# Optimization experiments

Hardware: AMD Instinct MI355X
Metric: run time of the kernel (lower is better)

## Reference

```python
import jax, jax.numpy as jnp
import numpy as np

N = 8192
D_IN = 512
HID = 1024
EMB = 64
N_EFF = 2
N_CLASSES = 16
MARGIN = 0.01


def setup_inputs() -> dict:
    key = jax.random.key(0)
    ks = jax.random.split(key, 10)
    data = jax.random.normal(ks[0], (N, D_IN), dtype=jnp.float32)
    labels = jax.random.randint(ks[1], (N,), 0, N_CLASSES).astype(jnp.float32)
    x = jnp.concatenate([labels[:, None], data], axis=1)  # [N, 1+D_IN]

    def lin(k, fan_in, fan_out):
        return jax.random.normal(k, (fan_in, fan_out), dtype=jnp.float32) / np.sqrt(fan_in)

    return {
        "x": x,
        "W1": lin(ks[2], D_IN, HID), "b1": jnp.zeros((HID,), jnp.float32),
        "W2": lin(ks[3], HID, EMB), "b2": jnp.zeros((EMB,), jnp.float32),
        "W3": lin(ks[4], EMB, HID), "b3": jnp.zeros((HID,), jnp.float32),
        "W4": lin(ks[5], HID, D_IN), "b4": jnp.zeros((D_IN,), jnp.float32),
    }


def reference(x, W1, b1, W2, b2, W3, b3, W4, b4):
    labels = x[:, 0]
    data = x[:, 1:]

    # encoder / decoder (tanh MLP autoencoder)
    embedding = jnp.tanh(data @ W1 + b1) @ W2 + b2          # [N, EMB]
    decoded = jnp.tanh(embedding @ W3 + b3) @ W4 + b4       # [N, D_IN]

    conserved = embedding[:, N_EFF:]                        # [N, C]
    n_conserved = conserved.shape[1]

    # labels.expand + unique(return_inverse) on row-replicated labels is
    # equivalent to comparing the labels directly.
    lbl = labels.astype(jnp.int32)
    Y = lbl[:, None] != lbl[None, :]                        # [N, N] bool

    # D_mean[i,j] = mean_d (c_i - c_j)^2, via Gram-matrix algebra (one pass,
    # no [N,N,C] intermediate).
    sq = jnp.sum(conserved * conserved, axis=1)             # [N]
    gram = conserved @ conserved.T                          # [N, N]
    D_mean = jnp.maximum(sq[:, None] + sq[None, :] - 2.0 * gram, 0.0) / n_conserved

    Yf = Y.astype(D_mean.dtype)
    n_diff = jnp.sum(Yf)
    C_sim = jnp.sum(Yf * D_mean) / (n_diff + 1.0)
    C_diff = jnp.sum((1.0 - Yf) * jnp.maximum(0.0, MARGIN - D_mean)) / (
        (D_mean.shape[0] * D_mean.shape[1] - n_diff) + 1.0)

    return decoded, C_sim, C_diff
```

## Files before the change

kernel.cpp:

```cpp
#include <hip/hip_runtime.h>
#include <stdint.h>

#define NROWS 8192
#define DIN   512
#define HIDN  1024
#define EMBN  64
#define NCONS 62
#define NCLS  16
#define MARGINF 0.01f
#define NREP  16

typedef unsigned short u16;
typedef __attribute__((ext_vector_type(8))) short short8;
typedef __attribute__((ext_vector_type(4))) float floatx4;

__device__ __forceinline__ u16 f32_to_bf16(float f) {
  union { float f; uint32_t u; } x; x.f = f;
  uint32_t u = x.u;
  uint32_t r = (u + 0x7FFFu + ((u >> 16) & 1u)) >> 16;
  return (u16)r;
}

__device__ __forceinline__ float bf16_to_f32(u16 h) {
  union { uint32_t u; float f; } x; x.u = (uint32_t)h << 16;
  return x.f;
}

__device__ __forceinline__ float fast_tanh(float x) {
  float xc = fminf(fmaxf(x, -10.f), 10.f);
  float e = __expf(2.f * xc);
  return (e - 1.f) * __builtin_amdgcn_rcpf(e + 1.f);
}

__device__ __forceinline__ void load_lds16(const u16* g, u16* l) {
  __builtin_amdgcn_global_load_lds(
      (const __attribute__((address_space(1))) void*)g,
      (__attribute__((address_space(3))) void*)l, 16, 0, 0);
}

__device__ __forceinline__ void pack_tile(const float* __restrict__ W,
                                          u16* __restrict__ Wp,
                                          int N, int KU, int t, int lane)
{
  const int r = lane >> 2, slot = lane & 3;
  const int c = slot ^ ((r >> 1) & 3);
  const int nt = t / KU, ku = t - nt * KU;
  const int n = nt * 16 + r;
  const int kb = ku * 32 + c * 8;
  short8 v;
#pragma unroll
  for (int j = 0; j < 8; ++j) v[j] = (short)f32_to_bf16(W[(size_t)(kb + j) * N + n]);
  *(short8*)(Wp + ((size_t)t * 64 + lane) * 8) = v;
}

__global__ __launch_bounds__(256)
void prep_all(const float* __restrict__ x,
              const float* __restrict__ W1, const float* __restrict__ W2,
              const float* __restrict__ W3, const float* __restrict__ W4,
              u16* __restrict__ A0p, u16* __restrict__ W1p,
              u16* __restrict__ W2p, u16* __restrict__ W3p,
              u16* __restrict__ W4p, float* __restrict__ slab,
              int* __restrict__ labels, int* __restrict__ hist32)
{
  __shared__ int hh[NCLS];
  const int b = blockIdx.x;
  const int tid = threadIdx.x;
  const int tl = tid >> 6, lane = tid & 63;
  if (b < 2048) {
    if (b < 32) {
      if (tid < NCLS) hh[tid] = 0;
      const int row = b * 256 + tid;
      const int lab = (int)x[(size_t)row * 513];
      labels[row] = lab;
      __syncthreads();
      atomicAdd(&hh[lab], 1);
      __syncthreads();
      if (tid < NCLS) hist32[b * NCLS + tid] = hh[tid];
    }
    const int t = b * 4 + tl;
    const int rt = t >> 4, ku = t & 15;
    const int r = lane & 15, q = lane >> 4;
    const float* src = x + (size_t)(rt * 16 + r) * 513 + 1 + ku * 32 + q * 8;
    short8 v;
#pragma unroll
    for (int j = 0; j < 8; ++j) v[j] = (short)f32_to_bf16(src[j]);
    *(short8*)(A0p + ((size_t)t * 64 + lane) * 8) = v;
  } else if (b < 2304) {
    pack_tile(W1, W1p, 1024, 16, (b - 2048) * 4 + tl, lane);
  } else if (b < 2336) {
    pack_tile(W2, W2p, 64, 32, (b - 2304) * 4 + tl, lane);
  } else if (b < 2368) {
    pack_tile(W3, W3p, 1024, 2, (b - 2336) * 4 + tl, lane);
  } else if (b < 2624) {
    pack_tile(W4, W4p, 512, 32, (b - 2368) * 4 + tl, lane);
  } else {
    float* dst = slab + (size_t)(b - 2624) * 4096;
    for (int i = tid; i < 4096; i += 256) dst[i] = 0.f;
  }
}

__global__ __launch_bounds__(512, 4)
void fused123(const u16* __restrict__ A0p, const u16* __restrict__ W1p,
              const float* __restrict__ b1, const u16* __restrict__ W2p,
              const float* __restrict__ b2, const u16* __restrict__ W3p,
              const float* __restrict__ b3,
              const int* __restrict__ labels, const int* __restrict__ hist32,
              int* __restrict__ offs, int* __restrict__ counts,
              int* __restrict__ idx,
              u16* __restrict__ Ebf, float* __restrict__ sqrow,
              float* __restrict__ vsumR, float* __restrict__ SsumR,
              u16* __restrict__ T)
{
  __shared__ u16 uni[16 * 1032];
  __shared__ u16 El[16 * 66];
  __shared__ float lv[NCLS][64];
  __shared__ float lsq[NCLS][64];
  __shared__ int colsum[NCLS], preblk[NCLS], scur[NCLS];

  const int tid = threadIdx.x;

  if (blockIdx.x < 16) {
    const int sb = blockIdx.x;
    if (tid < NCLS) {
      int s = 0, p = 0;
      for (int b2i = 0; b2i < 32; ++b2i) {
        const int h = hist32[b2i * NCLS + tid];
        s += h;
        if (b2i < sb * 2) p += h;
      }
      colsum[tid] = s;
      preblk[tid] = p;
    }
    __syncthreads();
    if (tid < NCLS) {
      int o = 0;
      for (int c = 0; c < tid; ++c) o += colsum[c];
      scur[tid] = o + preblk[tid];
      if (sb == 0) {
        counts[tid] = colsum[tid];
        offs[tid] = o;
        if (tid == NCLS - 1) offs[NCLS] = o + colsum[NCLS - 1];
      }
    }
    __syncthreads();
    {
      const int row = sb * 512 + tid;
      const int p = atomicAdd(&scur[labels[row]], 1);
      idx[p] = row;
    }
    return;
  }

  const int bx = blockIdx.x - 16;
  const int m0 = bx * 16;
  const int rep = blockIdx.x & (NREP - 1);
  const int w = tid >> 6, lane = tid & 63;
  const int quad = lane >> 4, l15 = lane & 15;
  const int lamb = l15 * 4 + (quad ^ ((l15 >> 1) & 3));

  for (int i = tid; i < NCLS * 64; i += 512) {
    ((float*)lv)[i] = 0.f; ((float*)lsq)[i] = 0.f;
  }

  u16* Hc = uni;
  float* Epart = (float*)uni;

  const u16* Wbase = W1p + (size_t)(w * 8) * 16 * 512 + lamb * 8;
  const u16* Abase = A0p + (size_t)(bx * 16) * 512 + lane * 8;

  floatx4 acc1[8];
#pragma unroll
  for (int jj = 0; jj < 8; ++jj) acc1[jj] = (floatx4){0.f, 0.f, 0.f, 0.f};

  short8 bfb[2][8];
  short8 afb[2];
  afb[0] = *(const short8*)(Abase);
#pragma unroll
  for (int jj = 0; jj < 8; ++jj)
    bfb[0][jj] = *(const short8*)(Wbase + (size_t)(jj * 16) * 512);

#pragma unroll
  for (int s = 0; s < 16; ++s) {
    const int cur = s & 1, nxt = cur ^ 1;
    if (s < 15) {
      afb[nxt] = *(const short8*)(Abase + (size_t)(s + 1) * 512);
#pragma unroll
      for (int jj = 0; jj < 8; ++jj)
        bfb[nxt][jj] = *(const short8*)(Wbase + (size_t)(jj * 16 + s + 1) * 512);
    }
#pragma unroll
    for (int jj = 0; jj < 8; ++jj)
      acc1[jj] = __builtin_amdgcn_mfma_f32_16x16x32_bf16(afb[cur], bfb[cur][jj], acc1[jj], 0, 0, 0);
  }

#pragma unroll
  for (int jj = 0; jj < 8; ++jj) {
    const int col = w * 128 + jj * 16 + l15;
    const float bv = b1[col];
#pragma unroll
    for (int r = 0; r < 4; ++r)
      Hc[(quad * 4 + r) * 1032 + col] = f32_to_bf16(fast_tanh(acc1[jj][r] + bv));
  }
  __syncthreads();

  floatx4 acc2[4];
#pragma unroll
  for (int nt = 0; nt < 4; ++nt) acc2[nt] = (floatx4){0.f, 0.f, 0.f, 0.f};

#pragma unroll
  for (int kk = 0; kk < 4; ++kk) {
    const int ku = w * 4 + kk;
    const short8 af = *(const short8*)(Hc + l15 * 1032 + ku * 32 + quad * 8);
#pragma unroll
    for (int nt = 0; nt < 4; ++nt) {
      const short8 bf = *(const short8*)(W2p + (size_t)(nt * 32 + ku) * 512 + lamb * 8);
      acc2[nt] = __builtin_amdgcn_mfma_f32_16x16x32_bf16(af, bf, acc2[nt], 0, 0, 0);
    }
  }
  __syncthreads();

#pragma unroll
  for (int nt = 0; nt < 4; ++nt)
#pragma unroll
    for (int r = 0; r < 4; ++r)
      Epart[((size_t)w * 16 + quad * 4 + r) * 64 + nt * 16 + l15] = acc2[nt][r];
  __syncthreads();

  {
    const float bv2 = b2[lane];
    for (int r = 0; r < 2; ++r) {
      const int row = w * 2 + r;
      const int grow = m0 + row;
      const int c = labels[grow];
      float acc = bv2;
#pragma unroll
      for (int p = 0; p < 8; ++p)
        acc += Epart[((size_t)p * 16 + row) * 64 + lane];
      const u16 h = f32_to_bf16(acc);
      Ebf[(size_t)grow * 64 + lane] = h;
      El[row * 66 + lane] = h;
      float v = bf16_to_f32(h);
      if (lane < 2) v = 0.f;
      const float v2 = v * v;
      atomicAdd(&lv[c][lane], v);
      atomicAdd(&lsq[c][lane], v2);
      float s = v2;
      for (int o = 32; o > 0; o >>= 1) s += __shfl_xor(s, o);
      if (lane == 0) sqrow[grow] = s;
    }
  }
  __syncthreads();

  for (int i = tid; i < NCLS * 64; i += 512) {
    const int c = i >> 6, k = i & 63;
    if (k >= 2) atomicAdd(&vsumR[rep * (NCLS * NCONS) + c * NCONS + k - 2], lv[c][k]);
  }
  if (tid < NCLS) {
    float s = 0.f;
    for (int k = 0; k < 64; ++k) s += lsq[tid][k];
    atomicAdd(&SsumR[rep * NCLS + tid], s);
  }

  floatx4 acc3[8];
#pragma unroll
  for (int jj = 0; jj < 8; ++jj) acc3[jj] = (floatx4){0.f, 0.f, 0.f, 0.f};

#pragma unroll
  for (int kk = 0; kk < 2; ++kk) {
    const short8 af = *(const short8*)(El + l15 * 66 + kk * 32 + quad * 8);
#pragma unroll
    for (int jj = 0; jj < 8; ++jj) {
      const int nt = w * 8 + jj;
      const short8 bf = *(const short8*)(W3p + (size_t)(nt * 2 + kk) * 512 + lamb * 8);
      acc3[jj] = __builtin_amdgcn_mfma_f32_16x16x32_bf16(af, bf, acc3[jj], 0, 0, 0);
    }
  }
#pragma unroll
  for (int jj = 0; jj < 8; ++jj) {
    const int col = w * 128 + jj * 16 + l15;
    const float bv3 = b3[col];
#pragma unroll
    for (int r = 0; r < 4; ++r)
      T[(size_t)(m0 + quad * 4 + r) * 1024 + col] =
          f32_to_bf16(fast_tanh(acc3[jj][r] + bv3));
  }
}

__global__ __launch_bounds__(256)
void tail(const u16* __restrict__ T, const u16* __restrict__ W4p,
          const float* __restrict__ b4, float* __restrict__ out,
          const u16* __restrict__ Ebf, const float* __restrict__ sqrow,
          const int* __restrict__ idx, const int* __restrict__ offs,
          float* __restrict__ pair_sum)
{
  __shared__ u16 uni[24576];
  const int tid = threadIdx.x, wave = tid >> 6, lane = tid & 63;
  const int quad = lane >> 4, l15 = lane & 15;

  if (blockIdx.x < 512) {
    u16* lA = uni;
    u16* lBb = uni + 16384;
    const int wm = wave >> 1, wn = wave & 1;
    const int xslot = (l15 >> 1) & 3;
    const int lin = blockIdx.x;
    const int n0 = (lin >> 6) * 64;
    const int m0 = (lin & 63) * 128;
    const int srow = lane >> 2;
    const int schunk = (lane & 3) ^ ((lane >> 3) & 3);

    auto stage = [&](int s, int buf) {
#pragma unroll
      for (int q = 0; q < 6; ++q) {
        const int u = wave + q * 4;
        if (u < 16) {
          const int rg = u >> 1, kh = u & 1;
          load_lds16(T + (size_t)(m0 + rg * 16 + srow) * 1024 + s * 64 + kh * 32 + schunk * 8,
                     lA + buf * 8192 + u * 512 + lane * 8);
        } else {
          const int v = u - 16, nt = v >> 1, kh = v & 1;
          load_lds16(W4p + (size_t)(((n0 >> 4) + nt) * 32 + s * 2 + kh) * 512 + lane * 8,
                     lBb + buf * 4096 + v * 512 + lane * 8);
        }
      }
    };

    stage(0, 0);
    __syncthreads();

    floatx4 acc[4][2];
#pragma unroll
    for (int i = 0; i < 4; ++i)
#pragma unroll
      for (int j = 0; j < 2; ++j) acc[i][j] = (floatx4){0.f, 0.f, 0.f, 0.f};

    for (int s = 0; s < 16; ++s) {
      const int p = s & 1;
      if (s < 15) stage(s + 1, 1 - p);
#pragma unroll
      for (int kk = 0; kk < 2; ++kk) {
        short8 af[4], bf[2];
#pragma unroll
        for (int i = 0; i < 4; ++i)
          af[i] = *(const short8*)(lA + p * 8192 + ((wm * 4 + i) * 2 + kk) * 512
                                   + l15 * 32 + ((quad ^ xslot) << 3));
#pragma unroll
        for (int j = 0; j < 2; ++j)
          bf[j] = *(const short8*)(lBb + p * 4096 + ((wn * 2 + j) * 2 + kk) * 512
                                   + l15 * 32 + ((quad ^ xslot) << 3));
#pragma unroll
        for (int i = 0; i < 4; ++i)
#pragma unroll
          for (int j = 0; j < 2; ++j)
            acc[i][j] = __builtin_amdgcn_mfma_f32_16x16x32_bf16(af[i], bf[j], acc[i][j], 0, 0, 0);
      }
      __syncthreads();
    }

#pragma unroll
    for (int i = 0; i < 4; ++i)
#pragma unroll
      for (int j = 0; j < 2; ++j) {
        const int col = n0 + wn * 32 + j * 16 + l15;
        const float bv = b4[col];
#pragma unroll
        for (int r = 0; r < 4; ++r) {
          const int row = m0 + wm * 64 + i * 16 + quad * 4 + r;
          out[(size_t)row * 512 + col] = acc[i][j][r] + bv;
        }
      }
    return;
  }

  const int q = blockIdx.x - 512;
  const int cls = q / 21;
  int p = q - cls * 21, ti = 0, cnt = 6;
  while (p >= cnt) { p -= cnt; ++ti; --cnt; }
  const int tj = ti + p;

  const int start = offs[cls];
  const int n = offs[cls + 1] - start;
  if (ti * 128 >= n || tj * 128 >= n) return;

  constexpr int LDA = 66;
  u16* Li = uni;
  u16* Lj = uni + 128 * LDA;
  float* sqI = (float*)(uni + 2 * 128 * LDA);
  float* sqJ = sqI + 128;
  float* red4 = sqJ + 128;

  for (int e = tid; e < 2048; e += 256) {
    const int t = e >> 10;
    const int row = (e >> 3) & 127;
    const int ch = e & 7;
    const int g = (t ? tj : ti) * 128 + row;
    short8 v = (short8)0;
    if (g < n) {
      v = *(const short8*)(Ebf + (size_t)idx[start + g] * EMBN + ch * 8);
      if (ch == 0) { v[0] = 0; v[1] = 0; }
    }
    *(short8*)((t ? Lj : Li) + row * LDA + ch * 8) = v;
  }
  {
    const int t = tid >> 7, row = tid & 127;
    const int g = (t ? tj : ti) * 128 + row;
    (t ? sqJ : sqI)[row] = (g < n) ? sqrow[idx[start + g]] : 0.f;
  }
  __syncthreads();

  const int wm = wave >> 1, wn = wave & 1;

  floatx4 acc[4][4];
#pragma unroll
  for (int i = 0; i < 4; ++i)
#pragma unroll
    for (int j = 0; j < 4; ++j) acc[i][j] = (floatx4){0.f, 0.f, 0.f, 0.f};

#pragma unroll
  for (int ks = 0; ks < 2; ++ks) {
    short8 af[4], bf[4];
#pragma unroll
    for (int i = 0; i < 4; ++i)
      af[i] = *(const short8*)(Li + (wm * 64 + i * 16 + l15) * LDA + ks * 32 + quad * 8);
#pragma unroll
    for (int j = 0; j < 4; ++j)
      bf[j] = *(const short8*)(Lj + (wn * 64 + j * 16 + l15) * LDA + ks * 32 + quad * 8);
#pragma unroll
    for (int i = 0; i < 4; ++i)
#pragma unroll
      for (int j = 0; j < 4; ++j)
        acc[i][j] = __builtin_amdgcn_mfma_f32_16x16x32_bf16(af[i], bf[j], acc[i][j], 0, 0, 0);
  }

  float local = 0.f;
#pragma unroll
  for (int i = 0; i < 4; ++i)
#pragma unroll
    for (int j = 0; j < 4; ++j)
#pragma unroll
      for (int r = 0; r < 4; ++r) {
        const int row = wm * 64 + i * 16 + quad * 4 + r;
        const int col = wn * 64 + j * 16 + l15;
        const int gi = ti * 128 + row, gj = tj * 128 + col;
        if (gi < n && gj < n && gi != gj) {
          const float D = (sqI[row] + sqJ[col] - 2.f * acc[i][j][r]) * (1.f / 62.f);
          local += fmaxf(0.f, MARGINF - D);
        }
      }
  if (ti < tj) local *= 2.f;

  for (int o = 32; o > 0; o >>= 1) local += __shfl_xor(local, o);
  if (lane == 0) red4[wave] = local;
  __syncthreads();
  if (tid == 0)
    atomicAdd(pair_sum, red4[0] + red4[1] + red4[2] + red4[3]);
}

__device__ __forceinline__ double block_reduce_d(double v, double* red, int tid) {
  red[tid] = v;
  __syncthreads();
  for (int st = 128; st > 0; st >>= 1) {
    if (tid < st) red[tid] += red[tid + st];
    __syncthreads();
  }
  const double r = red[0];
  __syncthreads();
  return r;
}

__global__ __launch_bounds__(256)
void finalize(const float* __restrict__ vsumR, const float* __restrict__ SsumR,
              const int* __restrict__ counts, const float* __restrict__ pair_sum,
              float* __restrict__ out2)
{
  const int tid = threadIdx.x;
  __shared__ double red[256];
  __shared__ float vtot[NCLS * NCONS];

  for (int i = tid; i < NCLS * NCONS; i += 256) {
    float s = 0.f;
    for (int r = 0; r < NREP; ++r) s += vsumR[r * (NCLS * NCONS) + i];
    vtot[i] = s;
  }
  __syncthreads();

  double v = 0.0;
  if (tid < NCLS) {
    float Sc = 0.f;
    for (int r = 0; r < NREP; ++r) Sc += SsumR[r * NCLS + tid];
    v = (double)Sc * (double)(NROWS - counts[tid]);
  }
  const double t1 = block_reduce_d(v, red, tid);

  v = 0.0;
  if (tid < NCLS) { const double nc = (double)counts[tid]; v = nc * nc; }
  const double n_same = block_reduce_d(v, red, tid);

  v = 0.0;
  for (int i = tid; i < NCLS * NCONS; i += 256) { const double w = vtot[i]; v += w * w; }
  const double t2 = block_reduce_d(v, red, tid);

  v = 0.0;
  if (tid < NCONS) {
    double Vk = 0.0;
    for (int c = 0; c < NCLS; ++c) Vk += (double)vtot[c * NCONS + tid];
    v = Vk * Vk;
  }
  const double t3 = block_reduce_d(v, red, tid);

  if (tid == 0) {
    const double n_diff = (double)NROWS * (double)NROWS - n_same;
    const double sim = 2.0 * t1 - 2.0 * (t3 - t2);
    const double C_sim = sim / 62.0 / (n_diff + 1.0);
    const double C_diff = ((double)pair_sum[0] + (double)NROWS * (double)MARGINF)
                          / (n_same + 1.0);
    out2[0] = (float)C_sim;
    out2[1] = (float)C_diff;
  }
}

extern "C" void kernel_launch(void* const* d_in, const int* in_sizes, int n_in,
                              void* d_out, int out_size, void* d_ws, size_t ws_size,
                              hipStream_t stream)
{
  const float* x  = (const float*)d_in[0];
  const float* W1 = (const float*)d_in[1];
  const float* b1 = (const float*)d_in[2];
  const float* W2 = (const float*)d_in[3];
  const float* b2 = (const float*)d_in[4];
  const float* W3 = (const float*)d_in[5];
  const float* b3 = (const float*)d_in[6];
  const float* W4 = (const float*)d_in[7];
  const float* b4 = (const float*)d_in[8];
  float* out = (float*)d_out;

  char* ws = (char*)d_ws;
  const size_t KB = 1024, MB = 1ull << 20;
  u16* A0p    = (u16*)(ws + 0);
  u16* W1p    = (u16*)(ws + 8 * MB);
  u16* W2p    = (u16*)(ws + 9 * MB);
  u16* W3p    = (u16*)(ws + 9 * MB + 128 * KB);
  u16* W4p    = (u16*)(ws + 9 * MB + 256 * KB);
  u16* Ebf    = (u16*)(ws + 18 * MB + 256 * KB);
  int* labels = (int*)(ws + 19 * MB + 256 * KB);
  int* idx    = (int*)(ws + 19 * MB + 288 * KB);
  float* sqrow = (float*)(ws + 19 * MB + 320 * KB);
  int* hist32 = (int*)(ws + 19 * MB + 352 * KB);
  float* slab = (float*)(ws + 19 * MB + 384 * KB);
  int*   counts  = (int*)slab;
  int*   offs    = counts + 16;
  float* psum    = slab + 64;
  float* SsumR   = slab + 128;
  float* vsumR   = slab + 512;
  u16* T      = (u16*)(ws + 20 * MB);
  (void)in_sizes; (void)n_in; (void)out_size; (void)ws_size;

  prep_all<<<dim3(2630), dim3(256), 0, stream>>>(x, W1, W2, W3, W4,
                                                 A0p, W1p, W2p, W3p, W4p,
                                                 slab, labels, hist32);
  fused123<<<dim3(528), dim3(512), 0, stream>>>(A0p, W1p, b1, W2p, b2, W3p, b3,
                                                labels, hist32, offs, counts, idx,
                                                Ebf, sqrow, vsumR, SsumR, T);
  tail<<<dim3(848), dim3(256), 0, stream>>>(T, W4p, b4, out,
                                            Ebf, sqrow, idx, offs, psum);
  finalize<<<dim3(1), dim3(256), 0, stream>>>(vsumR, SsumR, counts, psum,
                                              out + (size_t)NROWS * DIN);
}
```

Measured before the change: 157.1 us.

## Fuse decoder output GEMM into encoder kernel, keeping hidden tile in LDS

The fourth matmul (tanh hidden times W4) moves into the fused per-16-row block. The tanh activations now stay in shared memory instead of being written to a global T buffer and read back by a separate tail kernel. The pairwise-loss part becomes its own kernel. This drops the global round trip for T and one GEMM phase, but each block now streams all of W4 from global/L2 without LDS staging, so the fused kernel gets longer and reuses weights less.

Result: no change. 159.9 us (+1.8%).

```diff
diff --git a/kernel.cpp b/kernel.cpp
--- a/kernel.cpp
+++ b/kernel.cpp
@@ -30,12 +30,6 @@
   float xc = fminf(fmaxf(x, -10.f), 10.f);
   float e = __expf(2.f * xc);
   return (e - 1.f) * __builtin_amdgcn_rcpf(e + 1.f);
-}
-
-__device__ __forceinline__ void load_lds16(const u16* g, u16* l) {
-  __builtin_amdgcn_global_load_lds(
-      (const __attribute__((address_space(1))) void*)g,
-      (__attribute__((address_space(3))) void*)l, 16, 0, 0);
 }
 
 __device__ __forceinline__ void pack_tile(const float* __restrict__ W,
@@ -100,16 +94,17 @@
 }
 
 __global__ __launch_bounds__(512, 4)
-void fused123(const u16* __restrict__ A0p, const u16* __restrict__ W1p,
-              const float* __restrict__ b1, const u16* __restrict__ W2p,
-              const float* __restrict__ b2, const u16* __restrict__ W3p,
-              const float* __restrict__ b3,
-              const int* __restrict__ labels, const int* __restrict__ hist32,
-              int* __restrict__ offs, int* __restrict__ counts,
-              int* __restrict__ idx,
-              u16* __restrict__ Ebf, float* __restrict__ sqrow,
-              float* __restrict__ vsumR, float* __restrict__ SsumR,
-              u16* __restrict__ T)
+void fused1234(const u16* __restrict__ A0p, const u16* __restrict__ W1p,
+               const float* __restrict__ b1, const u16* __restrict__ W2p,
+               const float* __restrict__ b2, const u16* __restrict__ W3p,
+               const float* __restrict__ b3, const u16* __restrict__ W4p,
+               const float* __restrict__ b4,
+               const int* __restrict__ labels, const int* __restrict__ hist32,
+               int* __restrict__ offs, int* __restrict__ counts,
+               int* __restrict__ idx,
+               u16* __restrict__ Ebf, float* __restrict__ sqrow,
+               float* __restrict__ vsumR, float* __restrict__ SsumR,
+               float* __restrict__ out)
 {
   __shared__ u16 uni[16 * 1032];
   __shared__ u16 El[16 * 66];
@@ -164,6 +159,7 @@
 
   u16* Hc = uni;
   float* Epart = (float*)uni;
+  u16* Tl = uni;
 
   const u16* Wbase = W1p + (size_t)(w * 8) * 16 * 512 + lamb * 8;
   const u16* Abase = A0p + (size_t)(bx * 16) * 512 + lane * 8;
@@ -281,97 +277,55 @@
     const float bv3 = b3[col];
 #pragma unroll
     for (int r = 0; r < 4; ++r)
-      T[(size_t)(m0 + quad * 4 + r) * 1024 + col] =
-          f32_to_bf16(fast_tanh(acc3[jj][r] + bv3));
+      Tl[(quad * 4 + r) * 1032 + col] = f32_to_bf16(fast_tanh(acc3[jj][r] + bv3));
+  }
+  __syncthreads();
+
+  const u16* W4base = W4p + (size_t)(w * 4) * 32 * 512 + lamb * 8;
+
+  floatx4 acc4[4];
+#pragma unroll
+  for (int nt = 0; nt < 4; ++nt) acc4[nt] = (floatx4){0.f, 0.f, 0.f, 0.f};
+
+  short8 b4b[2][4];
+  short8 a4b[2];
+  a4b[0] = *(const short8*)(Tl + l15 * 1032 + quad * 8);
+#pragma unroll
+  for (int nt = 0; nt < 4; ++nt)
+    b4b[0][nt] = *(const short8*)(W4base + (size_t)(nt * 32) * 512);
+
+#pragma unroll
+  for (int ku = 0; ku < 32; ++ku) {
+    const int cur = ku & 1, nxt = cur ^ 1;
+    if (ku < 31) {
+      a4b[nxt] = *(const short8*)(Tl + l15 * 1032 + (ku + 1) * 32 + quad * 8);
+#pragma unroll
+      for (int nt = 0; nt < 4; ++nt)
+        b4b[nxt][nt] = *(const short8*)(W4base + (size_t)(nt * 32 + ku + 1) * 512);
+    }
+#pragma unroll
+    for (int nt = 0; nt < 4; ++nt)
+      acc4[nt] = __builtin_amdgcn_mfma_f32_16x16x32_bf16(a4b[cur], b4b[cur][nt], acc4[nt], 0, 0, 0);
+  }
+
+#pragma unroll
+  for (int nt = 0; nt < 4; ++nt) {
+    const int col = w * 64 + nt * 16 + l15;
+    const float bv4 = b4[col];
+#pragma unroll
+    for (int r = 0; r < 4; ++r) {
+      const int row = m0 + quad * 4 + r;
+      out[(size_t)row * 512 + col] = acc4[nt][r] + bv4;
+    }
   }
 }
 
 __global__ __launch_bounds__(256)
-void tail(const u16* __restrict__ T, const u16* __restrict__ W4p,
-          const float* __restrict__ b4, float* __restrict__ out,
-          const u16* __restrict__ Ebf, const float* __restrict__ sqrow,
-          const int* __restrict__ idx, const int* __restrict__ offs,
-          float* __restrict__ pair_sum)
+void pairwise_mfma(const u16* __restrict__ Ebf, const float* __restrict__ sqrow,
+                   const int* __restrict__ idx, const int* __restrict__ offs,
+                   float* __restrict__ pair_sum)
 {
-  __shared__ u16 uni[24576];
-  const int tid = threadIdx.x, wave = tid >> 6, lane = tid & 63;
-  const int quad = lane >> 4, l15 = lane & 15;
-
-  if (blockIdx.x < 512) {
-    u16* lA = uni;
-    u16* lBb = uni + 16384;
-    const int wm = wave >> 1, wn = wave & 1;
-    const int xslot = (l15 >> 1) & 3;
-    const int lin = blockIdx.x;
-    const int n0 = (lin >> 6) * 64;
-    const int m0 = (lin & 63) * 128;
-    const int srow = lane >> 2;
-    const int schunk = (lane & 3) ^ ((lane >> 3) & 3);
-
-    auto stage = [&](int s, int buf) {
-#pragma unroll
-      for (int q = 0; q < 6; ++q) {
-        const int u = wave + q * 4;
-        if (u < 16) {
-          const int rg = u >> 1, kh = u & 1;
-          load_lds16(T + (size_t)(m0 + rg * 16 + srow) * 1024 + s * 64 + kh * 32 + schunk * 8,
-                     lA + buf * 8192 + u * 512 + lane * 8);
-        } else {
-          const int v = u - 16, nt = v >> 1, kh = v & 1;
-          load_lds16(W4p + (size_t)(((n0 >> 4) + nt) * 32 + s * 2 + kh) * 512 + lane * 8,
-                     lBb + buf * 4096 + v * 512 + lane * 8);
-        }
-      }
-    };
-
-    stage(0, 0);
-    __syncthreads();
-
-    floatx4 acc[4][2];
-#pragma unroll
-    for (int i = 0; i < 4; ++i)
-#pragma unroll
-      for (int j = 0; j < 2; ++j) acc[i][j] = (floatx4){0.f, 0.f, 0.f, 0.f};
-
-    for (int s = 0; s < 16; ++s) {
-      const int p = s & 1;
-      if (s < 15) stage(s + 1, 1 - p);
-#pragma unroll
-      for (int kk = 0; kk < 2; ++kk) {
-        short8 af[4], bf[2];
-#pragma unroll
-        for (int i = 0; i < 4; ++i)
-          af[i] = *(const short8*)(lA + p * 8192 + ((wm * 4 + i) * 2 + kk) * 512
-                                   + l15 * 32 + ((quad ^ xslot) << 3));
-#pragma unroll
-        for (int j = 0; j < 2; ++j)
-          bf[j] = *(const short8*)(lBb + p * 4096 + ((wn * 2 + j) * 2 + kk) * 512
-                                   + l15 * 32 + ((quad ^ xslot) << 3));
-#pragma unroll
-        for (int i = 0; i < 4; ++i)
-#pragma unroll
-          for (int j = 0; j < 2; ++j)
-            acc[i][j] = __builtin_amdgcn_mfma_f32_16x16x32_bf16(af[i], bf[j], acc[i][j], 0, 0, 0);
-      }
-      __syncthreads();
-    }
-
-#pragma unroll
-    for (int i = 0; i < 4; ++i)
-#pragma unroll
-      for (int j = 0; j < 2; ++j) {
-        const int col = n0 + wn * 32 + j * 16 + l15;
-        const float bv = b4[col];
-#pragma unroll
-        for (int r = 0; r < 4; ++r) {
-          const int row = m0 + wm * 64 + i * 16 + quad * 4 + r;
-          out[(size_t)row * 512 + col] = acc[i][j][r] + bv;
-        }
-      }
-    return;
-  }
-
-  const int q = blockIdx.x - 512;
+  const int q = blockIdx.x;
   const int cls = q / 21;
   int p = q - cls * 21, ti = 0, cnt = 6;
   while (p >= cnt) { p -= cnt; ++ti; --cnt; }
@@ -382,11 +336,13 @@
   if (ti * 128 >= n || tj * 128 >= n) return;
 
   constexpr int LDA = 66;
-  u16* Li = uni;
-  u16* Lj = uni + 128 * LDA;
-  float* sqI = (float*)(uni + 2 * 128 * LDA);
-  float* sqJ = sqI + 128;
-  float* red4 = sqJ + 128;
+  __shared__ u16 Li[128 * LDA];
+  __shared__ u16 Lj[128 * LDA];
+  __shared__ float sqI[128], sqJ[128];
+  __shared__ float red4[4];
+
+  const int tid = threadIdx.x, wave = tid >> 6, lane = tid & 63;
+  const int quad = lane >> 4, l15 = lane & 15;
 
   for (int e = tid; e < 2048; e += 256) {
     const int t = e >> 10;
@@ -551,17 +507,16 @@
   float* psum    = slab + 64;
   float* SsumR   = slab + 128;
   float* vsumR   = slab + 512;
-  u16* T      = (u16*)(ws + 20 * MB);
   (void)in_sizes; (void)n_in; (void)out_size; (void)ws_size;
 
   prep_all<<<dim3(2630), dim3(256), 0, stream>>>(x, W1, W2, W3, W4,
                                                  A0p, W1p, W2p, W3p, W4p,
                                                  slab, labels, hist32);
-  fused123<<<dim3(528), dim3(512), 0, stream>>>(A0p, W1p, b1, W2p, b2, W3p, b3,
-                                                labels, hist32, offs, counts, idx,
-                                                Ebf, sqrow, vsumR, SsumR, T);
-  tail<<<dim3(848), dim3(256), 0, stream>>>(T, W4p, b4, out,
-                                            Ebf, sqrow, idx, offs, psum);
+  fused1234<<<dim3(528), dim3(512), 0, stream>>>(A0p, W1p, b1, W2p, b2, W3p, b3,
+                                                 W4p, b4,
+                                                 labels, hist32, offs, counts, idx,
+                                                 Ebf, sqrow, vsumR, SsumR, out);
+  pairwise_mfma<<<dim3(336), dim3(256), 0, stream>>>(Ebf, sqrow, idx, offs, psum);
   finalize<<<dim3(1), dim3(256), 0, stream>>>(vsumR, SsumR, counts, psum,
                                               out + (size_t)NROWS * DIN);
 }
```
